# Performance work log

Measured on AMD Instinct MI355X. Metric: run time of the kernel, lower is better.

Reference implementation:

```python
import jax, jax.numpy as jnp
import numpy as np

B, QL, DL, H = 16, 1024, 4096, 128


def setup_inputs() -> dict:
    key = jax.random.key(0)
    k1, k2, k3, k4, k5 = jax.random.split(key, 5)
    return {
        "query_input": jax.random.normal(k1, (B, QL, H), dtype=jnp.float32),
        "query_mask": jax.random.randint(k2, (B, QL), 0, 2, dtype=jnp.int32),
        "doc_input": jax.random.normal(k3, (B, DL, H), dtype=jnp.float32),
        "doc_mask": jax.random.randint(k4, (B, DL), 0, 2, dtype=jnp.int32),
        "sim_matrix": jax.random.normal(k5, (B, QL, DL), dtype=jnp.float32),
    }


def reference(query_input, query_mask, doc_input, doc_mask, sim_matrix):
    # query_input: (b, q, d); doc_input: (b, k, d); sim_matrix: (b, q, k)
    dim = query_input.shape[-1]
    scale = 1.0 / jnp.sqrt(jnp.asarray(dim, dtype=query_input.dtype))
    scores = jnp.einsum("bqd,bkd->bqk", query_input, doc_input) * scale
    # mask out padded doc positions (broadcast doc_mask over query axis)
    scores = jnp.where(doc_mask[:, None, :] == 0, jnp.asarray(-9999.0, scores.dtype), scores)
    attn = jax.nn.softmax(scores, axis=-1)  # (b, q, k)
    # sim-weighted reduction over doc axis, then sum over query axis
    query_atten_sim = jnp.sum(attn * sim_matrix, axis=-1)  # (b, q)
    return jnp.sum(query_atten_sim, axis=-1, keepdims=True)  # (b, 1)
```

## Files before the change

### kernel.cpp

```cpp
#include <hip/hip_runtime.h>
#include <hip/hip_bf16.h>

#define NB 16
#define QL 1024
#define DLEN 4096
#define HD 128

#define NSL 128
#define NIT (QL / 16)
#define WLDS (3 * 6144)

typedef __attribute__((ext_vector_type(8))) short short8;
typedef __attribute__((ext_vector_type(4))) float f32x4;

__device__ __forceinline__ short bf16_of(float x) {
  union { __hip_bfloat16 h; short s; } u;
  u.h = __float2bfloat16(x);
  return u.s;
}

__device__ __forceinline__ short8 cvt8(float4 a, float4 b) {
  short8 r;
  r[0] = bf16_of(a.x); r[1] = bf16_of(a.y); r[2] = bf16_of(a.z); r[3] = bf16_of(a.w);
  r[4] = bf16_of(b.x); r[5] = bf16_of(b.y); r[6] = bf16_of(b.z); r[7] = bf16_of(b.w);
  return r;
}

__global__ __launch_bounds__(256) void cvt_q(const float* __restrict__ in,
                                             short8* __restrict__ outw) {
  const size_t i = (size_t)blockIdx.x * 256 + threadIdx.x;
  const float* p = in + i * 8;
  outw[i] = cvt8(*(const float4*)p, *(const float4*)(p + 4));
}

__global__ __launch_bounds__(512) void atten_cross(
    const __hip_bfloat16* __restrict__ qbf, const float* __restrict__ doc,
    const int* __restrict__ dmask, const float* __restrict__ sim,
    float2* __restrict__ ws) {
  const int flat = blockIdx.x;
  const int b = flat & 15;
  const int g = flat >> 4;
  const int tid = threadIdx.x;
  const int w = tid >> 6;
  const int lane = tid & 63;
  const int grp = lane >> 4;
  const int li = lane & 15;
  const int slice = g * 8 + w;
  const int k0 = slice * 32;

  __shared__ char lds[8 * WLDS];
  const int wbase = w * WLDS;

  const float* dsrc = doc + ((size_t)b * DLEN + k0 + li) * HD + grp * 8;
  short8 afr[2][4];
#pragma unroll
  for (int kt = 0; kt < 2; ++kt)
#pragma unroll
    for (int cc = 0; cc < 4; ++cc) {
      const float* p = dsrc + (size_t)kt * 16 * HD + cc * 32;
      afr[kt][cc] = cvt8(*(const float4*)p, *(const float4*)(p + 4));
    }
  const int* mp = dmask + (size_t)b * DLEN + k0 + grp * 4;
  const int4 mk0 = *(const int4*)(mp);
  const int4 mk1 = *(const int4*)(mp + 16);

  const char* gq = (const char*)qbf + ((size_t)b * QL) * (HD * 2);
  const char* gsim = (const char*)sim + ((size_t)b * QL) * (DLEN * 4) + (size_t)k0 * 4;
  const char* qsrcj[4];
#pragma unroll
  for (int j = 0; j < 4; ++j) {
    const int row = j * 4 + (lane >> 4), x = (lane & 15) * 16;
    qsrcj[j] = gq + (size_t)row * 256 + (x ^ ((row & 7) << 4));
  }
  const char* ssrcj[2];
#pragma unroll
  for (int j = 0; j < 2; ++j) {
    const int row = j * 8 + (lane >> 3), x = (lane & 7) * 16;
    ssrcj[j] = gsim + (size_t)row * (DLEN * 4) + (x ^ ((row & 7) << 4));
  }

#define STAGE(it, pan)                                                         \
  {                                                                            \
    const size_t qo = (size_t)(it) * (16 * HD * 2);                            \
    const size_t so = (size_t)(it) * (16 * DLEN * 4);                          \
    _Pragma("unroll") for (int j = 0; j < 4; ++j)                              \
      __builtin_amdgcn_global_load_lds(                                        \
          (const __attribute__((address_space(1))) void*)(qsrcj[j] + qo),      \
          (__attribute__((address_space(3))) void*)(lds + wbase + (pan)*6144 + j*1024 + lane*16), \
          16, 0, 0);                                                           \
    _Pragma("unroll") for (int j = 0; j < 2; ++j)                              \
      __builtin_amdgcn_global_load_lds(                                        \
          (const __attribute__((address_space(1))) void*)(ssrcj[j] + so),      \
          (__attribute__((address_space(3))) void*)(lds + wbase + (pan)*6144 + 4096 + j*1024 + lane*16), \
          16, 0, 0);                                                           \
  }

  constexpr float scale = 0.088388347648318447f;
  const int qxor = (li & 7) << 4;
  const int mm0[4] = {mk0.x, mk0.y, mk0.z, mk0.w};
  const int mm1[4] = {mk1.x, mk1.y, mk1.z, mk1.w};

  STAGE(0, 0);
  STAGE(1, 1);

#pragma unroll 1
  for (int it = 0; it < NIT; ++it) {
    if (it == 0)      asm volatile("s_waitcnt vmcnt(6)" ::: "memory");
    else if (it == 1) asm volatile("s_waitcnt vmcnt(7)" ::: "memory");
    else              asm volatile("s_waitcnt vmcnt(8)" ::: "memory");
    __builtin_amdgcn_sched_barrier(0);

    {
      const int nx = (it + 2 < NIT) ? it + 2 : NIT - 1;
      STAGE(nx, (it + 2) % 3);
    }

    const char* qp = lds + wbase + (it % 3) * 6144;
    const char* sp = qp + 4096;

    short8 bfrag[4];
#pragma unroll
    for (int cc = 0; cc < 4; ++cc)
      bfrag[cc] = *(const short8*)(qp + li * 256 + ((grp * 16 + cc * 64) ^ qxor));

    float l = 0.f, nn = 0.f;
#pragma unroll
    for (int kt = 0; kt < 2; ++kt) {
      f32x4 acc = {0.f, 0.f, 0.f, 0.f};
      acc = __builtin_amdgcn_mfma_f32_16x16x32_bf16(afr[kt][0], bfrag[0], acc, 0, 0, 0);
      acc = __builtin_amdgcn_mfma_f32_16x16x32_bf16(afr[kt][1], bfrag[1], acc, 0, 0, 0);
      acc = __builtin_amdgcn_mfma_f32_16x16x32_bf16(afr[kt][2], bfrag[2], acc, 0, 0, 0);
      acc = __builtin_amdgcn_mfma_f32_16x16x32_bf16(afr[kt][3], bfrag[3], acc, 0, 0, 0);
      const f32x4 sv = *(const f32x4*)(sp + li * 128 + ((kt * 64 + grp * 16) ^ qxor));
#pragma unroll
      for (int r = 0; r < 4; ++r) {
        float e = __expf(acc[r] * scale);
        e = (kt ? mm1[r] : mm0[r]) ? e : 0.f;
        l += e;
        nn = fmaf(e, sv[r], nn);
      }
    }

    l += __shfl_xor(l, 16, 64); l += __shfl_xor(l, 32, 64);
    nn += __shfl_xor(nn, 16, 64); nn += __shfl_xor(nn, 32, 64);
    if (lane < 16)
      ws[((size_t)slice * NB + b) * QL + it * 16 + li] = make_float2(l, nn);
  }
#undef STAGE
}

__global__ __launch_bounds__(256) void finish(const float2* __restrict__ ws,
                                              float* __restrict__ out) {
  const int b = blockIdx.x;
  const int qg = blockIdx.y;
  const int t = threadIdx.x;
  const int q = qg * 64 + (t & 63);
  const int sg = t >> 6;

  float l = 0.f, n = 0.f;
#pragma unroll 8
  for (int s = sg * 32; s < sg * 32 + 32; ++s) {
    const float2 v = ws[((size_t)s * NB + b) * QL + q];
    l += v.x;
    n += v.y;
  }
  __shared__ float rl[4][64], rn[4][64];
  rl[sg][t & 63] = l;
  rn[sg][t & 63] = n;
  __syncthreads();
  if (t < 64) {
    const float lt = rl[0][t] + rl[1][t] + rl[2][t] + rl[3][t];
    const float nt = rn[0][t] + rn[1][t] + rn[2][t] + rn[3][t];
    float v = nt / lt;
#pragma unroll
    for (int m = 32; m >= 1; m >>= 1) v += __shfl_xor(v, m, 64);
    if (t == 0) atomicAdd(out + b, v);
  }
}

extern "C" void kernel_launch(void* const* d_in, const int* in_sizes, int n_in,
                              void* d_out, int out_size, void* d_ws, size_t ws_size,
                              hipStream_t stream) {
  const float* qin = (const float*)d_in[0];
  const float* doc = (const float*)d_in[2];
  const int* dmask = (const int*)d_in[3];
  const float* sim = (const float*)d_in[4];
  float* out = (float*)d_out;

  float2* ws = (float2*)d_ws;
  short8* qbf = (short8*)((char*)d_ws + (size_t)128 * NB * QL * 8);

  hipMemsetAsync(out, 0, (size_t)out_size * sizeof(float), stream);

  const size_t q_elems = (size_t)NB * QL * HD;
  cvt_q<<<q_elems / (8 * 256), 256, 0, stream>>>(qin, qbf);

  dim3 grid(NB * 16);
  atten_cross<<<grid, 512, 0, stream>>>((const __hip_bfloat16*)qbf, doc,
                                        dmask, sim, ws);
  finish<<<dim3(NB, 16), 256, 0, stream>>>(ws, out);
}
```

Measured before the change: 93.78 us.

## Load query fragments directly to registers and double-buffer 32-row steps

Query bf16 fragments now go from global memory straight into registers, double-buffered across two register sets, instead of being staged through LDS. Only sim tiles still use the LDS ring. Each iteration now handles 32 query rows, and blocks shrink to 256 threads with a 2-blocks-per-CU launch bound, keeping the same 128 doc slices. This removes LDS traffic and LDS reads for Q and doubles the work per wait, at the cost of higher VGPR pressure and more uncoalesced direct global loads of Q.

Measured after the change: 116.0 us. 1.24x slower.

```diff
diff --git a/kernel.cpp b/kernel.cpp
--- a/kernel.cpp
+++ b/kernel.cpp
@@ -6,9 +6,9 @@
 #define DLEN 4096
 #define HD 128
 
-#define NSL 128
-#define NIT (QL / 16)
-#define WLDS (3 * 6144)
+#define KCB 128
+#define NKC (DLEN / KCB)
+#define NIT (QL / 32)
 
 typedef __attribute__((ext_vector_type(8))) short short8;
 typedef __attribute__((ext_vector_type(4))) float f32x4;
@@ -18,7 +18,6 @@
   u.h = __float2bfloat16(x);
   return u.s;
 }
-
 __device__ __forceinline__ short8 cvt8(float4 a, float4 b) {
   short8 r;
   r[0] = bf16_of(a.x); r[1] = bf16_of(a.y); r[2] = bf16_of(a.z); r[3] = bf16_of(a.w);
@@ -33,23 +32,24 @@
   outw[i] = cvt8(*(const float4*)p, *(const float4*)(p + 4));
 }
 
-__global__ __launch_bounds__(512) void atten_cross(
+__global__ __launch_bounds__(256, 2) void atten_cross(
     const __hip_bfloat16* __restrict__ qbf, const float* __restrict__ doc,
     const int* __restrict__ dmask, const float* __restrict__ sim,
     float2* __restrict__ ws) {
   const int flat = blockIdx.x;
   const int b = flat & 15;
-  const int g = flat >> 4;
+  const int kc = flat >> 4;
   const int tid = threadIdx.x;
   const int w = tid >> 6;
   const int lane = tid & 63;
   const int grp = lane >> 4;
   const int li = lane & 15;
-  const int slice = g * 8 + w;
-  const int k0 = slice * 32;
-
-  __shared__ char lds[8 * WLDS];
-  const int wbase = w * WLDS;
+  const int k0 = kc * KCB + w * 32;
+
+  __shared__ char lds[4 * 3 * 4096];
+  char* ring = lds + w * 12288;
+
+  constexpr float scale = 0.088388347648318447f;
 
   const float* dsrc = doc + ((size_t)b * DLEN + k0 + li) * HD + grp * 8;
   short8 afr[2][4];
@@ -60,93 +60,116 @@
       const float* p = dsrc + (size_t)kt * 16 * HD + cc * 32;
       afr[kt][cc] = cvt8(*(const float4*)p, *(const float4*)(p + 4));
     }
-  const int* mp = dmask + (size_t)b * DLEN + k0 + grp * 4;
-  const int4 mk0 = *(const int4*)(mp);
-  const int4 mk1 = *(const int4*)(mp + 16);
-
-  const char* gq = (const char*)qbf + ((size_t)b * QL) * (HD * 2);
-  const char* gsim = (const char*)sim + ((size_t)b * QL) * (DLEN * 4) + (size_t)k0 * 4;
-  const char* qsrcj[4];
+  int mm[2][4];
+  {
+    const int* mp = dmask + (size_t)b * DLEN + k0 + grp * 4;
+    const int4 a = *(const int4*)(mp);
+    const int4 c = *(const int4*)(mp + 16);
+    mm[0][0] = a.x; mm[0][1] = a.y; mm[0][2] = a.z; mm[0][3] = a.w;
+    mm[1][0] = c.x; mm[1][1] = c.y; mm[1][2] = c.z; mm[1][3] = c.w;
+  }
+
+  const char* ssrc[4];
+  int sdd[4];
 #pragma unroll
   for (int j = 0; j < 4; ++j) {
-    const int row = j * 4 + (lane >> 4), x = (lane & 15) * 16;
-    qsrcj[j] = gq + (size_t)row * 256 + (x ^ ((row & 7) << 4));
-  }
-  const char* ssrcj[2];
-#pragma unroll
-  for (int j = 0; j < 2; ++j) {
-    const int row = j * 8 + (lane >> 3), x = (lane & 7) * 16;
-    ssrcj[j] = gsim + (size_t)row * (DLEN * 4) + (x ^ ((row & 7) << 4));
-  }
-
-#define STAGE(it, pan)                                                         \
+    const int row = j * 8 + (lane >> 3);
+    ssrc[j] = (const char*)sim + ((size_t)b * QL + row) * (DLEN * 4) +
+              (size_t)kc * 512 + (size_t)w * 128 +
+              (((lane & 7) * 16) ^ ((((lane >> 3) & 7)) << 4));
+    sdd[j] = j * 1024 + lane * 16;
+  }
+
+#define STAGE(it, buf)                                                         \
   {                                                                            \
-    const size_t qo = (size_t)(it) * (16 * HD * 2);                            \
-    const size_t so = (size_t)(it) * (16 * DLEN * 4);                          \
+    const size_t adv = (size_t)(it) * (32 * DLEN * 4);                         \
     _Pragma("unroll") for (int j = 0; j < 4; ++j)                              \
       __builtin_amdgcn_global_load_lds(                                        \
-          (const __attribute__((address_space(1))) void*)(qsrcj[j] + qo),      \
-          (__attribute__((address_space(3))) void*)(lds + wbase + (pan)*6144 + j*1024 + lane*16), \
+          (const __attribute__((address_space(1))) void*)(ssrc[j] + adv),      \
+          (__attribute__((address_space(3))) void*)(ring + (buf) * 4096 + sdd[j]), \
           16, 0, 0);                                                           \
-    _Pragma("unroll") for (int j = 0; j < 2; ++j)                              \
-      __builtin_amdgcn_global_load_lds(                                        \
-          (const __attribute__((address_space(1))) void*)(ssrcj[j] + so),      \
-          (__attribute__((address_space(3))) void*)(lds + wbase + (pan)*6144 + 4096 + j*1024 + lane*16), \
-          16, 0, 0);                                                           \
-  }
-
-  constexpr float scale = 0.088388347648318447f;
-  const int qxor = (li & 7) << 4;
-  const int mm0[4] = {mk0.x, mk0.y, mk0.z, mk0.w};
-  const int mm1[4] = {mk1.x, mk1.y, mk1.z, mk1.w};
+  }
+
+  const __hip_bfloat16* qsrc = qbf + ((size_t)b * QL + li) * HD + grp * 8;
+
+#define LOADBQ(it, dst)                                                        \
+  {                                                                            \
+    const __hip_bfloat16* qp_ = qsrc + (size_t)(it) * (32 * HD);               \
+    _Pragma("unroll") for (int qh = 0; qh < 2; ++qh)                           \
+      _Pragma("unroll") for (int cc = 0; cc < 4; ++cc)                         \
+        dst[qh * 4 + cc] =                                                     \
+            *(const short8*)(qp_ + (size_t)qh * 16 * HD + cc * 32);            \
+  }
+
+#define PIN(a)                                                                 \
+  asm volatile("" : "+v"(a[0]), "+v"(a[1]), "+v"(a[2]), "+v"(a[3]),            \
+                    "+v"(a[4]), "+v"(a[5]), "+v"(a[6]), "+v"(a[7]));
+
+  const int qswz = (li & 7) << 4;
+
+#define CONSUME(it, bq)                                                        \
+  {                                                                            \
+    const char* sp = ring + ((it) % 3) * 4096;                                 \
+    _Pragma("unroll") for (int qh = 0; qh < 2; ++qh) {                         \
+      float l = 0.f, nn = 0.f;                                                 \
+      _Pragma("unroll") for (int kt = 0; kt < 2; ++kt) {                       \
+        f32x4 acc = {0.f, 0.f, 0.f, 0.f};                                      \
+        _Pragma("unroll") for (int cc = 0; cc < 4; ++cc)                       \
+          acc = __builtin_amdgcn_mfma_f32_16x16x32_bf16(afr[kt][cc],           \
+                                                        bq[qh * 4 + cc], acc, 0, 0, 0); \
+        const f32x4 sv = *(const f32x4*)(sp + (qh * 16 + li) * 128 +           \
+                                         ((kt * 64 + grp * 16) ^ qswz));       \
+        _Pragma("unroll") for (int r = 0; r < 4; ++r) {                        \
+          float e = __expf(acc[r] * scale);                                    \
+          e = mm[kt][r] ? e : 0.f;                     \
+          l += e;                                                              \
+          nn = fmaf(e, sv[r], nn);                                             \
+        }                                                                      \
+      }                                                                        \
+      l += __shfl_xor(l, 16, 64); l += __shfl_xor(l, 32, 64);                  \
+      nn += __shfl_xor(nn, 16, 64); nn += __shfl_xor(nn, 32, 64);              \
+      if (lane < 16)                                                           \
+        ws[((size_t)(kc * 4 + w) * NB + b) * QL + (it) * 32 + qh * 16 + li] =  \
+            make_float2(l, nn);                                                \
+    }                                                                          \
+    asm volatile("" ::: "memory");        \
+  }
+
+  short8 bqA[8], bqB[8];
 
   STAGE(0, 0);
   STAGE(1, 1);
+  LOADBQ(0, bqA);
+  PIN(bqA);
 
 #pragma unroll 1
-  for (int it = 0; it < NIT; ++it) {
-    if (it == 0)      asm volatile("s_waitcnt vmcnt(6)" ::: "memory");
-    else if (it == 1) asm volatile("s_waitcnt vmcnt(7)" ::: "memory");
-    else              asm volatile("s_waitcnt vmcnt(8)" ::: "memory");
-    __builtin_amdgcn_sched_barrier(0);
-
+  for (int p = 0; p < NIT / 2; ++p) {
+    const int itE = 2 * p, itO = 2 * p + 1;
     {
-      const int nx = (it + 2 < NIT) ? it + 2 : NIT - 1;
-      STAGE(nx, (it + 2) % 3);
+      const int st = (itE + 2 < NIT) ? itE + 2 : NIT - 1;
+      STAGE(st, (itE + 2) % 3);
+      LOADBQ(itE + 1, bqB);
+      PIN(bqB);
+      if (itE == 0) asm volatile("s_waitcnt vmcnt(12)" ::: "memory");
+      else          asm volatile("s_waitcnt vmcnt(14)" ::: "memory");
+      __builtin_amdgcn_sched_barrier(0);
+      CONSUME(itE, bqA);
     }
-
-    const char* qp = lds + wbase + (it % 3) * 6144;
-    const char* sp = qp + 4096;
-
-    short8 bfrag[4];
-#pragma unroll
-    for (int cc = 0; cc < 4; ++cc)
-      bfrag[cc] = *(const short8*)(qp + li * 256 + ((grp * 16 + cc * 64) ^ qxor));
-
-    float l = 0.f, nn = 0.f;
-#pragma unroll
-    for (int kt = 0; kt < 2; ++kt) {
-      f32x4 acc = {0.f, 0.f, 0.f, 0.f};
-      acc = __builtin_amdgcn_mfma_f32_16x16x32_bf16(afr[kt][0], bfrag[0], acc, 0, 0, 0);
-      acc = __builtin_amdgcn_mfma_f32_16x16x32_bf16(afr[kt][1], bfrag[1], acc, 0, 0, 0);
-      acc = __builtin_amdgcn_mfma_f32_16x16x32_bf16(afr[kt][2], bfrag[2], acc, 0, 0, 0);
-      acc = __builtin_amdgcn_mfma_f32_16x16x32_bf16(afr[kt][3], bfrag[3], acc, 0, 0, 0);
-      const f32x4 sv = *(const f32x4*)(sp + li * 128 + ((kt * 64 + grp * 16) ^ qxor));
-#pragma unroll
-      for (int r = 0; r < 4; ++r) {
-        float e = __expf(acc[r] * scale);
-        e = (kt ? mm1[r] : mm0[r]) ? e : 0.f;
-        l += e;
-        nn = fmaf(e, sv[r], nn);
-      }
+    {
+      const int st = (itO + 2 < NIT) ? itO + 2 : NIT - 1;
+      const int bl = (itO + 1 < NIT) ? itO + 1 : NIT - 1;
+      STAGE(st, (itO + 2) % 3);
+      LOADBQ(bl, bqA);
+      PIN(bqA);
+      asm volatile("s_waitcnt vmcnt(14)" ::: "memory");
+      __builtin_amdgcn_sched_barrier(0);
+      CONSUME(itO, bqB);
     }
-
-    l += __shfl_xor(l, 16, 64); l += __shfl_xor(l, 32, 64);
-    nn += __shfl_xor(nn, 16, 64); nn += __shfl_xor(nn, 32, 64);
-    if (lane < 16)
-      ws[((size_t)slice * NB + b) * QL + it * 16 + li] = make_float2(l, nn);
   }
 #undef STAGE
+#undef LOADBQ
+#undef PIN
+#undef CONSUME
 }
 
 __global__ __launch_bounds__(256) void finish(const float2* __restrict__ ws,
@@ -193,10 +216,10 @@
   hipMemsetAsync(out, 0, (size_t)out_size * sizeof(float), stream);
 
   const size_t q_elems = (size_t)NB * QL * HD;
-  cvt_q<<<q_elems / (8 * 256), 256, 0, stream>>>(qin, qbf);
-
-  dim3 grid(NB * 16);
-  atten_cross<<<grid, 512, 0, stream>>>((const __hip_bfloat16*)qbf, doc,
+  cvt_q<<<q_elems / (8 * 256), 256, 0, stream>>>(qin, (short8*)qbf);
+
+  dim3 grid(NB * NKC);
+  atten_cross<<<grid, 256, 0, stream>>>((const __hip_bfloat16*)qbf, doc,
                                         dmask, sim, ws);
   finish<<<dim3(NB, 16), 256, 0, stream>>>(ws, out);
 }
```
